# Optimization experiments

Measured on AMD Instinct MI355X. Metric: run time of the kernel, lower is better.

Reference implementation:

```python
import jax, jax.numpy as jnp
import numpy as np

D_MODEL, D_STATE, EXPAND, V, BATCH, L = 32, 16, 2, 19, 32, 256
D_INNER = EXPAND * D_MODEL          # 64
DT_RANK = 2                          # ceil(d_model/16)
N_NODES = BATCH * V                  # 608


def setup_inputs() -> dict:
    key = jax.random.key(0)
    ks = jax.random.split(key, 16)
    # 32 fully-connected directed 19-vertex graphs (no self loops), block-diagonal batching
    ii, jj = np.nonzero(~np.eye(V, dtype=bool))
    offs = (np.arange(BATCH) * V)[:, None]
    src = (ii[None, :] + offs).reshape(-1)
    dst = (jj[None, :] + offs).reshape(-1)
    edge_index = jnp.asarray(np.stack([src, dst]), dtype=jnp.int32)  # (2, 10944)
    E = edge_index.shape[1]
    # dt_proj bias init (inverse softplus of dt in [dt_min, dt_max]), as in the torch module
    dt = jnp.exp(jax.random.uniform(ks[6], (D_INNER,)) * (np.log(0.1) - np.log(0.001)) + np.log(0.001))
    dt = jnp.maximum(dt, 1e-4)
    inv_dt = dt + jnp.log(-jnp.expm1(-dt))
    s = 0.05
    return {
        'x_in': jax.random.normal(ks[0], (N_NODES, L, D_MODEL), jnp.float32),
        'edge_index': edge_index,
        'edge_weight': jax.random.uniform(ks[1], (E,), jnp.float32, 0.1, 1.0),
        'in_proj_w': jax.random.normal(ks[2], (2 * D_INNER, D_MODEL), jnp.float32) * s,
        'x_proj_w': jax.random.normal(ks[3], (DT_RANK + 2 * D_STATE, D_INNER), jnp.float32) * s,
        'dt_proj_w': jax.random.uniform(ks[4], (D_INNER, DT_RANK), jnp.float32, -DT_RANK ** -0.5, DT_RANK ** -0.5),
        'dt_proj_b': inv_dt,
        'A_log': jnp.log(jnp.broadcast_to(jnp.arange(1, D_STATE + 1, dtype=jnp.float32), (D_INNER, D_STATE))),
        'D_param': jnp.ones((D_INNER,), jnp.float32),
        'out_proj_w': jax.random.normal(ks[5], (D_MODEL, D_INNER), jnp.float32) * s,
        'gA_w': jax.random.normal(ks[7], (D_INNER, D_INNER), jnp.float32) * s,
        'gA_b': jnp.zeros((D_INNER,), jnp.float32),
        'gB_w': jax.random.normal(ks[8], (D_INNER, D_INNER), jnp.float32) * s,
        'gB_b': jnp.zeros((D_INNER,), jnp.float32),
        'gC_w': jax.random.normal(ks[9], (D_INNER, D_INNER), jnp.float32) * s,
        'gC_b': jnp.zeros((D_INNER,), jnp.float32),
    }


def reference(x_in, edge_index, edge_weight, in_proj_w, x_proj_w, dt_proj_w,
              dt_proj_b, A_log, D_param, out_proj_w,
              gA_w, gA_b, gB_w, gB_b, gC_w, gC_b):
    n_nodes, seqlen, _ = x_in.shape
    dt_rank = dt_proj_w.shape[1]
    d_state = A_log.shape[1]

    # --- GCN symmetric normalization with self loops (weight 1), as in PyG GCNConv ---
    loop = jnp.arange(n_nodes, dtype=edge_index.dtype)
    src = jnp.concatenate([edge_index[0], loop])
    dst = jnp.concatenate([edge_index[1], loop])
    w = jnp.concatenate([edge_weight, jnp.ones((n_nodes,), edge_weight.dtype)])
    deg = jax.ops.segment_sum(w, dst, num_segments=n_nodes)
    dinv = jax.lax.rsqrt(jnp.maximum(deg, 1e-12))
    norm = w * dinv[src] * dinv[dst]  # (E+n,)

    def gcn_vec(f, W, b):  # f: (V, d)
        h = f @ W.T
        return jax.ops.segment_sum(norm[:, None] * h[src], dst, num_segments=n_nodes) + b

    def gcn_state(f, W, b):  # f: (V, d, n); linear acts on the d (feature) axis
        h = jnp.einsum('vdn,ed->ven', f, W)
        agg = jax.ops.segment_sum(norm[:, None, None] * h[src], dst, num_segments=n_nodes)
        return agg + b[None, :, None]

    # --- projections ---
    xz = jnp.einsum('vld,ed->vle', x_in, in_proj_w)            # (V, L, 2*d_inner)
    x, z = jnp.split(xz, 2, axis=-1)                           # (V, L, d_inner)
    x_dbl = jnp.einsum('vld,ed->vle', x, x_proj_w)
    dtr, Bm, Cm = jnp.split(x_dbl, [dt_rank, dt_rank + d_state], axis=-1)
    dt = jax.nn.softplus(jnp.einsum('vlr,dr->vld', dtr, dt_proj_w) + dt_proj_b)  # (V, L, d_inner)
    A = -jnp.exp(A_log)                                        # (d_inner, d_state)

    # --- selective scan with per-timestep GCN on state (A), input (B), output (C) ---
    def step(s, inp):
        dt_t, B_t, C_t, u_t, z_t = inp  # (V,d), (V,n), (V,n), (V,d), (V,d)
        dA = jnp.exp(dt_t[:, :, None] * A[None])               # (V, d, n)
        sA = gcn_state(s, gA_w, gA_b)
        uB = gcn_vec(u_t, gB_w, gB_b)                          # (V, d)
        s_new = sA * dA + uB[:, :, None] * (dt_t[:, :, None] * B_t[:, None, :])
        sC = gcn_state(s_new, gC_w, gC_b)
        y_t = jnp.einsum('vdn,vn->vd', sC, C_t) + D_param * u_t
        y_t = y_t * jax.nn.silu(z_t)
        return s_new, y_t

    xs = (dt.transpose(1, 0, 2), Bm.transpose(1, 0, 2), Cm.transpose(1, 0, 2),
          x.transpose(1, 0, 2), z.transpose(1, 0, 2))
    s0 = jnp.zeros((n_nodes, A_log.shape[0], d_state), x_in.dtype)
    _, ys = jax.lax.scan(step, s0, xs)                         # (L, V, d_inner)
    y = ys.transpose(1, 0, 2)                                  # (V, L, d_inner)
    return jnp.einsum('vle,oe->vlo', y, out_proj_w)            # (V, L, d_model)
```

## Files before the change

kernel.cpp:

```cpp
#include <hip/hip_runtime.h>
#include <hip/hip_bf16.h>

typedef __hip_bfloat16 bf16;
typedef unsigned short ushort_t;
typedef __attribute__((ext_vector_type(8))) short bf16x8;
typedef __attribute__((ext_vector_type(4))) float f32x4;

#define NV_   19
#define NB_   32
#define NN_   608
#define LL_   256
#define NE_   10944
#define NROWS (NN_*LL_)
#define NTOT  (NROWS*64)
#define NBC   (NROWS*16)

__device__ __forceinline__ float b2f(bf16 x){ return __bfloat162float(x); }
__device__ __forceinline__ bf16 f2b(float x){ return __float2bfloat16(x); }
__device__ __forceinline__ unsigned short f2bs(float x){
  union { float f; unsigned u; } c; c.f = x;
  unsigned r = c.u + 0x7FFFu + ((c.u >> 16) & 1u);
  return (unsigned short)(r >> 16);
}
__device__ __forceinline__ float busf(unsigned short s){
  union { unsigned u; float f; } c; c.u = ((unsigned)s) << 16; return c.f;
}
__device__ __forceinline__ unsigned pkrn(float a, float b){
  union { __hip_bfloat162 h2; unsigned u; } c;
  float2 t; t.x = a; t.y = b;
  c.h2 = __float22bfloat162_rn(t);
  return c.u;
}
__device__ __forceinline__ float blo(unsigned u){
  union { unsigned x; float f; } c; c.x = u << 16; return c.f;
}
__device__ __forceinline__ float bhi(unsigned u){
  union { unsigned x; float f; } c; c.x = u & 0xffff0000u; return c.f;
}
__device__ __forceinline__ float softplusf(float x){
  return fmaxf(x, 0.f) + log1pf(expf(-fabsf(x)));
}

__global__ void k_deg(const int* __restrict__ ei, const float* __restrict__ ew,
                      float* __restrict__ deg){
  int i = blockIdx.x*256 + threadIdx.x;
  if (i < NN_) atomicAdd(&deg[i], 1.0f);
  if (i < NE_) atomicAdd(&deg[ei[NE_ + i]], ew[i]);
}

__global__ void k_dinv(const float* __restrict__ deg, float* __restrict__ dinv,
                       float* __restrict__ M){
  int v = blockIdx.x*256 + threadIdx.x;
  if (v >= NN_) return;
  float r = rsqrtf(fmaxf(deg[v], 1e-12f));
  dinv[v] = r;
  int b = v / NV_, lv = v - b*NV_;
  M[(b*NV_ + lv)*NV_ + lv] = r*r;
}

__global__ void k_edges(const int* __restrict__ ei, const float* __restrict__ ew,
                        const float* __restrict__ dinv, float* __restrict__ M){
  int i = blockIdx.x*256 + threadIdx.x;
  if (i >= NE_) return;
  int s = ei[i], d = ei[NE_ + i];
  float nrm = ew[i] * dinv[s] * dinv[d];
  int b = d / NV_;
  atomicAdd(&M[(b*NV_ + (d - b*NV_))*NV_ + (s - b*NV_)], nrm);
}

__global__ __launch_bounds__(256)
void k_proj(const float* __restrict__ xin, const float* __restrict__ inw,
            const float* __restrict__ xpw,
            bf16* __restrict__ u, bf16* __restrict__ zs,
            float* __restrict__ dtr, bf16* __restrict__ Bm, bf16* __restrict__ Cm){
  __shared__ float inT[32*129];
  __shared__ float xpT[64*35];
  __shared__ float xl[2][4][32];
  __shared__ float xh[2][4][64];
  int tid = threadIdx.x;
  for (int i = tid; i < 128*32; i += 256){
    int e = i >> 5, d = i & 31;
    inT[d*129 + e] = inw[i];
  }
  for (int i = tid; i < 34*64; i += 256){
    int j = i >> 6, e = i & 63;
    xpT[e*35 + j] = xpw[i];
  }
  int w = tid >> 6, lane = tid & 63;
  for (int rg = 0; rg < 32; rg++){
    int p = rg & 1;
    int r = (blockIdx.x*32 + rg)*4 + w;
    if (lane < 32) xl[p][w][lane] = xin[r*32 + lane];
    __syncthreads();
    float a0 = 0.f, a1 = 0.f;
    #pragma unroll
    for (int d = 0; d < 32; d++){
      float xv = xl[p][w][d];
      a0 = fmaf(inT[d*129 + lane], xv, a0);
      a1 = fmaf(inT[d*129 + 64 + lane], xv, a1);
    }
    int node = r >> 8, l = r & 255;
    long ob = (long)l*NN_ + node;
    u[ob*64 + lane] = f2b(a0);
    zs[ob*64 + lane] = f2b(a1 / (1.f + expf(-a1)));
    xh[p][w][lane] = a0;
    __syncthreads();
    if (lane < 34){
      float acc = 0.f;
      #pragma unroll
      for (int e = 0; e < 64; e++) acc = fmaf(xpT[e*35 + lane], xh[p][w][e], acc);
      if (lane < 2)       dtr[ob*2 + lane] = acc;
      else if (lane < 18) Bm[ob*16 + lane - 2] = f2b(acc);
      else                Cm[ob*16 + lane - 18] = f2b(acc);
    }
  }
}

__global__ __launch_bounds__(256)
void k_ub(const bf16* __restrict__ u, const float* __restrict__ gBw,
          const float* __restrict__ gBb, const float* __restrict__ Mg,
          const float* __restrict__ dtrg, const float* __restrict__ dtw,
          const float* __restrict__ dtb,
          bf16* __restrict__ uBsp, bf16* __restrict__ spb){
  __shared__ float wT[64*65];
  __shared__ float uL[19*64];
  __shared__ float hL[20*64];
  __shared__ float MLP[640];
  int b = blockIdx.x & 31, tc = blockIdx.x >> 5;
  int tid = threadIdx.x;
  for (int i = tid; i < 4096; i += 256){
    int e = i >> 6, d = i & 63;
    wT[d*65 + e] = gBw[i];
  }
  for (int i = tid; i < 640; i += 256){
    int vp = i >> 5, c = i & 31, g = c >> 3, k = c & 7;
    int v = g + 4*k;
    MLP[i] = (k < 5 && vp < 19 && v < 19) ? Mg[b*361 + v*19 + vp] : 0.f;
  }
  int vg = tid >> 6, e = tid & 63;
  int v0 = vg, v1 = vg+4, v2 = vg+8, v3 = vg+12, v4 = vg+16;
  int v4c = (vg == 3) ? 18 : v4;
  float w0e = dtw[e*2], w1e = dtw[e*2 + 1], dbe = dtb[e], bbe = gBb[e];
  const float* mlb = MLP + vg*8;
  for (int tt = 0; tt < 8; tt++){
    int t = tc*8 + tt;
    long rb = (long)t*NN_ + b*19;
    const bf16* up = u + rb*64;
    for (int i = tid; i < 1216; i += 256) uL[i] = b2f(up[i]);
    __syncthreads();
    float h0=0.f,h1=0.f,h2=0.f,h3=0.f,h4=0.f;
    #pragma unroll
    for (int d = 0; d < 64; d++){
      float wv = wT[d*65 + e];
      h0 = fmaf(wv, uL[v0*64 + d], h0);
      h1 = fmaf(wv, uL[v1*64 + d], h1);
      h2 = fmaf(wv, uL[v2*64 + d], h2);
      h3 = fmaf(wv, uL[v3*64 + d], h3);
      h4 = fmaf(wv, uL[v4c*64 + d], h4);
    }
    hL[v0*64 + e] = h0; hL[v1*64 + e] = h1; hL[v2*64 + e] = h2;
    hL[v3*64 + e] = h3; hL[v4*64 + e] = h4;
    __syncthreads();
    float acc0=bbe, acc1=bbe, acc2=bbe, acc3=bbe, acc4=bbe;
    #pragma unroll
    for (int vp = 0; vp < 20; vp++){
      float hv = hL[vp*64 + e];
      float4 m4 = *(const float4*)(mlb + vp*32);
      float  m5 = mlb[vp*32 + 4];
      acc0 = fmaf(m4.x, hv, acc0); acc1 = fmaf(m4.y, hv, acc1);
      acc2 = fmaf(m4.z, hv, acc2); acc3 = fmaf(m4.w, hv, acc3);
      acc4 = fmaf(m5,  hv, acc4);
    }
    float2 q0 = *(const float2*)(dtrg + (rb+v0)*2);
    float2 q1 = *(const float2*)(dtrg + (rb+v1)*2);
    float2 q2 = *(const float2*)(dtrg + (rb+v2)*2);
    float2 q3 = *(const float2*)(dtrg + (rb+v3)*2);
    float2 q4 = *(const float2*)(dtrg + (rb+v4c)*2);
    float s0 = softplusf(fmaf(q0.x, w0e, fmaf(q0.y, w1e, dbe)));
    float s1 = softplusf(fmaf(q1.x, w0e, fmaf(q1.y, w1e, dbe)));
    float s2 = softplusf(fmaf(q2.x, w0e, fmaf(q2.y, w1e, dbe)));
    float s3 = softplusf(fmaf(q3.x, w0e, fmaf(q3.y, w1e, dbe)));
    float s4 = softplusf(fmaf(q4.x, w0e, fmaf(q4.y, w1e, dbe)));
    bf16* op = uBsp + rb*64;
    bf16* sp = spb + rb*64;
    op[v0*64 + e] = f2b(acc0*s0);  sp[v0*64 + e] = f2b(s0);
    op[v1*64 + e] = f2b(acc1*s1);  sp[v1*64 + e] = f2b(s1);
    op[v2*64 + e] = f2b(acc2*s2);  sp[v2*64 + e] = f2b(s2);
    op[v3*64 + e] = f2b(acc3*s3);  sp[v3*64 + e] = f2b(s3);
    if (vg != 3){ op[v4*64 + e] = f2b(acc4*s4); sp[v4*64 + e] = f2b(s4); }
    __syncthreads();
  }
}

__global__ __launch_bounds__(1024)
void k_scan(const float* __restrict__ Mg,
            const bf16* __restrict__ spbg, const bf16* __restrict__ uBspg,
            const bf16* __restrict__ Bg, const bf16* __restrict__ Cg,
            const float* __restrict__ gAw, const float* __restrict__ gAb,
            const float* __restrict__ gCw, const float* __restrict__ gCb,
            const float* __restrict__ Alog, bf16* __restrict__ yp)
{
  __shared__ __align__(16) short Sb[2*32*72];
  __shared__ __align__(16) short H0[2*64*40];
  __shared__ __align__(16) short H1[2*64*40];
  __shared__ __align__(16) short Yx[2][32*64];
  int b = blockIdx.x >> 3, npair = blockIdx.x & 7;
  int tid = threadIdx.x;
  int team = tid >> 9;
  int tw   = (tid >> 6) & 7;
  int lane = tid & 63;
  int l15  = lane & 15, quad = lane >> 4;
  int n = npair*2 + team;
  int mt = tw >> 2, nt = tw & 3;
  int et = tw >> 1, vt = tw & 1;

  for (int i = tid; i < 2304; i += 1024) ((int*)Sb)[i] = 0;

  bf16x8 wa0, wa1, wc0, wc1;
  {
    #define PACK8(dst, p) { float4 lo_ = *(const float4*)(p); \
      float4 hi_ = *(const float4*)((p)+4); \
      dst[0]=(short)f2bs(lo_.x); dst[1]=(short)f2bs(lo_.y); \
      dst[2]=(short)f2bs(lo_.z); dst[3]=(short)f2bs(lo_.w); \
      dst[4]=(short)f2bs(hi_.x); dst[5]=(short)f2bs(hi_.y); \
      dst[6]=(short)f2bs(hi_.z); dst[7]=(short)f2bs(hi_.w); }
    const float* wrA = gAw + (16*nt + l15)*64 + quad*8;
    const float* wrC = gCw + (16*nt + l15)*64 + quad*8;
    PACK8(wa0, wrA) PACK8(wa1, wrA + 32)
    PACK8(wc0, wrC) PACK8(wc1, wrC + 32)
    #undef PACK8
  }
  bf16x8 mf;
  {
    const float* mb = Mg + b*361;
    int vr = 16*vt + l15; if (vr > 18) vr = 18;
    #pragma unroll
    for (int j = 0; j < 8; j++){
      int vp = quad*8 + j;
      mf[j] = (short)f2bs((vp < 19) ? mb[vr*19 + vp] : 0.f);
    }
  }
  int e0 = 16*et + 4*quad;
  int v_ = 16*vt + l15;
  int vc = (v_ > 18) ? 18 : v_;
  bool vok = (v_ < 19);
  float4 gab = *(const float4*)(gAb + e0);
  float4 gcb = *(const float4*)(gCb + e0);
  float An0 = -__expf(Alog[(e0+0)*16 + n]);
  float An1 = -__expf(Alog[(e0+1)*16 + n]);
  float An2 = -__expf(Alog[(e0+2)*16 + n]);
  float An3 = -__expf(Alog[(e0+3)*16 + n]);

  short* Sme  = Sb + team*32*72;
  short* H0me = H0 + team*64*40;
  short* H1me = H1 + team*64*40;
  int nodeBase = b*19;
  const short* prS  = Sme + (16*mt + l15)*72 + quad*8;
  short*       pwH0 = H0me + (16*nt + l15)*40 + 16*mt + quad*4;
  short*       pwH1 = H1me + (16*nt + l15)*40 + 16*mt + quad*4;
  const short* arH0 = H0me + (16*et + l15)*40 + quad*8;
  const short* arH1 = H1me + (16*et + l15)*40 + quad*8;
  short*       swS  = Sme + v_*72 + e0;

  long row0 = (long)nodeBase + vc;
  const ushort_t* psp = (const ushort_t*)spbg  + row0*64 + e0;
  const ushort_t* pub = (const ushort_t*)uBspg + row0*64 + e0;
  const ushort_t* pB  = (const ushort_t*)Bg + row0*16 + n;
  const ushort_t* pC  = (const ushort_t*)Cg + row0*16 + n;
  uint2 sp_n = *(const uint2*)psp;
  uint2 ub_n = *(const uint2*)pub;
  float B_n = busf(*pB);
  float C_b2 = busf(*pC);
  float C_a = 0.f;
  float pyo0=0.f,pyo1=0.f,pyo2=0.f,pyo3=0.f;
  float pyn0=0.f,pyn1=0.f,pyn2=0.f,pyn3=0.f;

  __syncthreads();
  {
    bf16x8 a0 = *(const bf16x8*)prS;
    bf16x8 a1 = *(const bf16x8*)(prS + 32);
    f32x4 p = {0.f,0.f,0.f,0.f};
    p = __builtin_amdgcn_mfma_f32_16x16x32_bf16(a0, wa0, p, 0,0,0);
    p = __builtin_amdgcn_mfma_f32_16x16x32_bf16(a1, wa1, p, 0,0,0);
    uint2 h; h.x = pkrn(p[0], p[1]); h.y = pkrn(p[2], p[3]);
    *(uint2*)pwH0 = h;
  }
  __syncthreads();

  for (int t = 0; t < 256; t++){
    uint2 sp_u = sp_n, ub_u = ub_n; float B_u = B_n;
    psp += NN_*64; pub += NN_*64; pB += NN_*16; pC += NN_*16;
    sp_n = *(const uint2*)psp;
    ub_n = *(const uint2*)pub;
    B_n = busf(*pB);
    float C_t = busf(*pC);
    bf16x8 hf0 = *(const bf16x8*)arH0;
    bf16x8 hf1 = *(const bf16x8*)arH1;
    {
      f32x4 qa = {gab.x, gab.y, gab.z, gab.w};
      qa = __builtin_amdgcn_mfma_f32_16x16x32_bf16(hf0, mf, qa, 0,0,0);
      float dA0 = __expf(blo(sp_u.x)*An0);
      float dA1 = __expf(bhi(sp_u.x)*An1);
      float dA2 = __expf(blo(sp_u.y)*An2);
      float dA3 = __expf(bhi(sp_u.y)*An3);
      float x0 = fmaf(qa[0], dA0, blo(ub_u.x)*B_u);
      float x1 = fmaf(qa[1], dA1, bhi(ub_u.x)*B_u);
      float x2 = fmaf(qa[2], dA2, blo(ub_u.y)*B_u);
      float x3 = fmaf(qa[3], dA3, bhi(ub_u.y)*B_u);
      uint2 sv; sv.x = pkrn(x0, x1); sv.y = pkrn(x2, x3);
      *(uint2*)swS = sv;
    }
    if (team == 0 && t >= 2 && vok){
      uint2 yv = *(const uint2*)(&Yx[t & 1][v_*64 + e0]);
      uint2 ov;
      ov.x = pkrn(pyo0 + blo(yv.x), pyo1 + bhi(yv.x));
      ov.y = pkrn(pyo2 + blo(yv.y), pyo3 + bhi(yv.y));
      *(uint2*)(yp + (((long)npair*256 + (t-2))*NN_ + nodeBase + v_)*64 + e0) = ov;
    }
    if (t >= 1){
      f32x4 qc = {gcb.x, gcb.y, gcb.z, gcb.w};
      qc = __builtin_amdgcn_mfma_f32_16x16x32_bf16(hf1, mf, qc, 0,0,0);
      float y0 = qc[0]*C_a, y1 = qc[1]*C_a, y2 = qc[2]*C_a, y3 = qc[3]*C_a;
      if (team == 1){
        uint2 yv; yv.x = pkrn(y0, y1); yv.y = pkrn(y2, y3);
        *(uint2*)(&Yx[(t-1) & 1][v_*64 + e0]) = yv;
      } else {
        pyo0 = pyn0; pyo1 = pyn1; pyo2 = pyn2; pyo3 = pyn3;
        pyn0 = y0; pyn1 = y1; pyn2 = y2; pyn3 = y3;
      }
    }
    C_a = C_b2; C_b2 = C_t;
    __syncthreads();
    {
      bf16x8 a0 = *(const bf16x8*)prS;
      bf16x8 a1 = *(const bf16x8*)(prS + 32);
      f32x4 p = {0.f,0.f,0.f,0.f};
      p = __builtin_amdgcn_mfma_f32_16x16x32_bf16(a0, wc0, p, 0,0,0);
      p = __builtin_amdgcn_mfma_f32_16x16x32_bf16(a1, wc1, p, 0,0,0);
      uint2 h; h.x = pkrn(p[0], p[1]); h.y = pkrn(p[2], p[3]);
      *(uint2*)pwH1 = h;
      f32x4 r = {0.f,0.f,0.f,0.f};
      r = __builtin_amdgcn_mfma_f32_16x16x32_bf16(a0, wa0, r, 0,0,0);
      r = __builtin_amdgcn_mfma_f32_16x16x32_bf16(a1, wa1, r, 0,0,0);
      uint2 g; g.x = pkrn(r[0], r[1]); g.y = pkrn(r[2], r[3]);
      *(uint2*)pwH0 = g;
    }
    __syncthreads();
  }
  {
    bf16x8 hf1 = *(const bf16x8*)arH1;
    f32x4 qc = {gcb.x, gcb.y, gcb.z, gcb.w};
    qc = __builtin_amdgcn_mfma_f32_16x16x32_bf16(hf1, mf, qc, 0,0,0);
    float y0 = qc[0]*C_a, y1 = qc[1]*C_a, y2 = qc[2]*C_a, y3 = qc[3]*C_a;
    if (team == 1){
      uint2 yv; yv.x = pkrn(y0, y1); yv.y = pkrn(y2, y3);
      *(uint2*)(&Yx[1][v_*64 + e0]) = yv;
    } else {
      pyo0 = pyn0; pyo1 = pyn1; pyo2 = pyn2; pyo3 = pyn3;
      pyn0 = y0; pyn1 = y1; pyn2 = y2; pyn3 = y3;
    }
  }
  __syncthreads();
  if (team == 0 && vok){
    uint2 yv = *(const uint2*)(&Yx[0][v_*64 + e0]);
    uint2 ov;
    ov.x = pkrn(pyo0 + blo(yv.x), pyo1 + bhi(yv.x));
    ov.y = pkrn(pyo2 + blo(yv.y), pyo3 + bhi(yv.y));
    *(uint2*)(yp + (((long)npair*256 + 254)*NN_ + nodeBase + v_)*64 + e0) = ov;
    uint2 yw = *(const uint2*)(&Yx[1][v_*64 + e0]);
    uint2 o2;
    o2.x = pkrn(pyn0 + blo(yw.x), pyn1 + bhi(yw.x));
    o2.y = pkrn(pyn2 + blo(yw.y), pyn3 + bhi(yw.y));
    *(uint2*)(yp + (((long)npair*256 + 255)*NN_ + nodeBase + v_)*64 + e0) = o2;
  }
}

__global__ __launch_bounds__(256)
void k_final(const bf16* __restrict__ yp, const bf16* __restrict__ u,
             const bf16* __restrict__ zs, const float* __restrict__ Dp,
             const float* __restrict__ ow, float* __restrict__ out)
{
  __shared__ float oT[64*33];
  __shared__ float yl[2][4][64];
  int tid = threadIdx.x;
  for (int i = tid; i < 32*64; i += 256){
    int o = i >> 6, e = i & 63;
    oT[e*33 + o] = ow[i];
  }
  int w = tid >> 6, lane = tid & 63;
  float dpl = Dp[lane];
  for (int rg = 0; rg < 16; rg++){
    int p = rg & 1;
    long r = (long)(blockIdx.x*16 + rg)*4 + w;
    long base = r*64;
    float y = dpl * b2f(u[base + lane]);
    #pragma unroll
    for (int q = 0; q < 8; q++) y += b2f(yp[(long)q*NTOT + base + lane]);
    y *= b2f(zs[base + lane]);
    yl[p][w][lane] = y;
    __syncthreads();
    if (lane < 32){
      float acc = 0.f;
      #pragma unroll
      for (int e = 0; e < 64; e++) acc = fmaf(oT[e*33 + lane], yl[p][w][e], acc);
      int t = (int)(r / NN_), node = (int)(r - (long)t*NN_);
      out[((long)node*256 + t)*32 + lane] = acc;
    }
  }
}

extern "C" void kernel_launch(void* const* d_in, const int* in_sizes, int n_in,
                              void* d_out, int out_size, void* d_ws, size_t ws_size,
                              hipStream_t stream)
{
  (void)in_sizes; (void)n_in; (void)out_size; (void)ws_size;
  const float* xin = (const float*)d_in[0];
  const int*   ei  = (const int*)  d_in[1];
  const float* ew  = (const float*)d_in[2];
  const float* inw = (const float*)d_in[3];
  const float* xpw = (const float*)d_in[4];
  const float* dtw = (const float*)d_in[5];
  const float* dtb = (const float*)d_in[6];
  const float* Alog= (const float*)d_in[7];
  const float* Dp  = (const float*)d_in[8];
  const float* ow  = (const float*)d_in[9];
  const float* gAw = (const float*)d_in[10];
  const float* gAb = (const float*)d_in[11];
  const float* gBw = (const float*)d_in[12];
  const float* gBb = (const float*)d_in[13];
  const float* gCw = (const float*)d_in[14];
  const float* gCb = (const float*)d_in[15];
  float* out = (float*)d_out;

  float* Mg   = (float*)d_ws;
  float* deg  = Mg + 11552;
  float* dinv = deg + 608;
  float* dtr  = dinv + 608;
  bf16*  u    = (bf16*)(dtr + 2*NROWS);
  bf16*  zs   = u + NTOT;
  bf16*  uBsp = zs + NTOT;
  bf16*  Bm   = uBsp + NTOT;
  bf16*  Cm   = Bm + NBC;
  bf16*  spb  = Cm + NBC;
  bf16*  yp   = spb + NTOT;

  hipMemsetAsync(d_ws, 0, (11552 + 608)*sizeof(float), stream);
  k_deg  <<<(NE_ + 255)/256, 256, 0, stream>>>(ei, ew, deg);
  k_dinv <<<(NN_ + 255)/256, 256, 0, stream>>>(deg, dinv, Mg);
  k_edges<<<(NE_ + 255)/256, 256, 0, stream>>>(ei, ew, dinv, Mg);
  k_proj <<<NROWS/(4*32), 256, 0, stream>>>(xin, inw, xpw, u, zs, dtr, Bm, Cm);
  k_ub   <<<32*32, 256, 0, stream>>>(u, gBw, gBb, Mg, dtr, dtw, dtb, uBsp, spb);
  k_scan <<<NB_*8, 1024, 0, stream>>>(Mg, spb, uBsp, Bm, Cm, gAw, gAb, gCw, gCb,
                                      Alog, yp);
  k_final<<<NROWS/(4*16), 256, 0, stream>>>(yp, u, zs, Dp, ow, out);
}
```

Baseline: 704.4 us.

## Shrink scan block to one wavefront per state index, removing intra-team barriers

The scan kernel drops from 1024 threads (8 waves per state index) to 128 threads, where one wavefront handles a whole state index and loops over all tiles in registers. Most shared-memory handoffs become intra-wave, leaving a single barrier per timestep for exchanging partial y sums between the two waves. The goal is to cut per-step synchronisation latency in the serial scan recurrence. The cost is far more MFMA and exp work per wave plus higher register pressure, with only 256 small blocks left to fill the GPU.

```diff
diff --git a/kernel.cpp b/kernel.cpp
--- a/kernel.cpp
+++ b/kernel.cpp
@@ -192,7 +192,7 @@
   }
 }
 
-__global__ __launch_bounds__(1024)
+__global__ __launch_bounds__(128, 1)
 void k_scan(const float* __restrict__ Mg,
             const bf16* __restrict__ spbg, const bf16* __restrict__ uBspg,
             const bf16* __restrict__ Bg, const bf16* __restrict__ Cg,
@@ -200,178 +200,212 @@
             const float* __restrict__ gCw, const float* __restrict__ gCb,
             const float* __restrict__ Alog, bf16* __restrict__ yp)
 {
-  __shared__ __align__(16) short Sb[2*32*72];
-  __shared__ __align__(16) short H0[2*64*40];
-  __shared__ __align__(16) short H1[2*64*40];
-  __shared__ __align__(16) short Yx[2][32*64];
-  int b = blockIdx.x >> 3, npair = blockIdx.x & 7;
-  int tid = threadIdx.x;
-  int team = tid >> 9;
-  int tw   = (tid >> 6) & 7;
-  int lane = tid & 63;
-  int l15  = lane & 15, quad = lane >> 4;
-  int n = npair*2 + team;
-  int mt = tw >> 2, nt = tw & 3;
-  int et = tw >> 1, vt = tw & 1;
-
-  for (int i = tid; i < 2304; i += 1024) ((int*)Sb)[i] = 0;
-
-  bf16x8 wa0, wa1, wc0, wc1;
-  {
-    #define PACK8(dst, p) { float4 lo_ = *(const float4*)(p); \
-      float4 hi_ = *(const float4*)((p)+4); \
-      dst[0]=(short)f2bs(lo_.x); dst[1]=(short)f2bs(lo_.y); \
-      dst[2]=(short)f2bs(lo_.z); dst[3]=(short)f2bs(lo_.w); \
-      dst[4]=(short)f2bs(hi_.x); dst[5]=(short)f2bs(hi_.y); \
-      dst[6]=(short)f2bs(hi_.z); dst[7]=(short)f2bs(hi_.w); }
-    const float* wrA = gAw + (16*nt + l15)*64 + quad*8;
-    const float* wrC = gCw + (16*nt + l15)*64 + quad*8;
-    PACK8(wa0, wrA) PACK8(wa1, wrA + 32)
-    PACK8(wc0, wrC) PACK8(wc1, wrC + 32)
-    #undef PACK8
-  }
-  bf16x8 mf;
+  __shared__ __align__(16) short Sb[2][32*72];
+  __shared__ __align__(16) short Hb0[2][64*40];
+  __shared__ __align__(16) short Hb1[2][64*40];
+  __shared__ __align__(16) unsigned Yex[2][2][64*12];
+
+  const int b = blockIdx.x >> 3, npair = blockIdx.x & 7;
+  const int tid = threadIdx.x;
+  const int team = tid >> 6;
+  const int lane = tid & 63;
+  const int l15 = lane & 15, quad = lane >> 4;
+  const int n = npair*2 + team;
+
+  for (int i = tid; i < 2560; i += 128) ((int*)Hb0)[i] = 0;
+
+  short* S  = Sb[team];
+  short* h0 = Hb0[team];
+  short* h1 = Hb1[team];
+
+  bf16x8 wa[4][2], wc[4][2];
+  #pragma unroll
+  for (int nt = 0; nt < 4; nt++){
+    const float* ra = gAw + (16*nt + l15)*64 + quad*8;
+    const float* rc = gCw + (16*nt + l15)*64 + quad*8;
+    #pragma unroll
+    for (int kc = 0; kc < 2; kc++){
+      #pragma unroll
+      for (int j = 0; j < 8; j++){
+        wa[nt][kc][j] = (short)f2bs(ra[kc*32 + j]);
+        wc[nt][kc][j] = (short)f2bs(rc[kc*32 + j]);
+      }
+    }
+  }
+  bf16x8 mfT[2];
   {
     const float* mb = Mg + b*361;
-    int vr = 16*vt + l15; if (vr > 18) vr = 18;
-    #pragma unroll
-    for (int j = 0; j < 8; j++){
-      int vp = quad*8 + j;
-      mf[j] = (short)f2bs((vp < 19) ? mb[vr*19 + vp] : 0.f);
-    }
-  }
-  int e0 = 16*et + 4*quad;
-  int v_ = 16*vt + l15;
-  int vc = (v_ > 18) ? 18 : v_;
-  bool vok = (v_ < 19);
-  float4 gab = *(const float4*)(gAb + e0);
-  float4 gcb = *(const float4*)(gCb + e0);
-  float An0 = -__expf(Alog[(e0+0)*16 + n]);
-  float An1 = -__expf(Alog[(e0+1)*16 + n]);
-  float An2 = -__expf(Alog[(e0+2)*16 + n]);
-  float An3 = -__expf(Alog[(e0+3)*16 + n]);
-
-  short* Sme  = Sb + team*32*72;
-  short* H0me = H0 + team*64*40;
-  short* H1me = H1 + team*64*40;
-  int nodeBase = b*19;
-  const short* prS  = Sme + (16*mt + l15)*72 + quad*8;
-  short*       pwH0 = H0me + (16*nt + l15)*40 + 16*mt + quad*4;
-  short*       pwH1 = H1me + (16*nt + l15)*40 + 16*mt + quad*4;
-  const short* arH0 = H0me + (16*et + l15)*40 + quad*8;
-  const short* arH1 = H1me + (16*et + l15)*40 + quad*8;
-  short*       swS  = Sme + v_*72 + e0;
-
-  long row0 = (long)nodeBase + vc;
-  const ushort_t* psp = (const ushort_t*)spbg  + row0*64 + e0;
-  const ushort_t* pub = (const ushort_t*)uBspg + row0*64 + e0;
-  const ushort_t* pB  = (const ushort_t*)Bg + row0*16 + n;
-  const ushort_t* pC  = (const ushort_t*)Cg + row0*16 + n;
-  uint2 sp_n = *(const uint2*)psp;
-  uint2 ub_n = *(const uint2*)pub;
-  float B_n = busf(*pB);
-  float C_b2 = busf(*pC);
-  float C_a = 0.f;
-  float pyo0=0.f,pyo1=0.f,pyo2=0.f,pyo3=0.f;
-  float pyn0=0.f,pyn1=0.f,pyn2=0.f,pyn3=0.f;
+    #pragma unroll
+    for (int vt = 0; vt < 2; vt++){
+      int v = 16*vt + l15;
+      #pragma unroll
+      for (int j = 0; j < 8; j++){
+        int vp = quad*8 + j;
+        mfT[vt][j] = (short)f2bs((v < 19 && vp < 19) ? mb[v*19 + vp] : 0.f);
+      }
+    }
+  }
+  float anv[4][4], gabv[4][4], gcbv[4][4];
+  #pragma unroll
+  for (int et = 0; et < 4; et++){
+    #pragma unroll
+    for (int r = 0; r < 4; r++){
+      int e = 16*et + 4*quad + r;
+      anv[et][r]  = -__expf(Alog[e*16 + n]);
+      gabv[et][r] = gAb[e];
+      gcbv[et][r] = gCb[e];
+    }
+  }
+
+  const int v1 = 16 + l15;
+  const int v1c = (v1 > 18) ? 18 : v1;
+  const long r0 = (long)b*19 + l15;
+  const long r1 = (long)b*19 + v1c;
+  const char* psp0 = (const char*)spbg  + r0*128 + quad*8;
+  const char* psp1 = (const char*)spbg  + r1*128 + quad*8;
+  const char* pub0 = (const char*)uBspg + r0*128 + quad*8;
+  const char* pub1 = (const char*)uBspg + r1*128 + quad*8;
+  const ushort_t* pB0 = (const ushort_t*)Bg + r0*16 + n;
+  const ushort_t* pB1 = (const ushort_t*)Bg + r1*16 + n;
+  const ushort_t* pC0 = (const ushort_t*)Cg + r0*16 + n;
+  const ushort_t* pC1 = (const ushort_t*)Cg + r1*16 + n;
+  bf16* py0 = yp + ((long)npair*256*NN_ + (long)b*19 + l15)*64;
+  bf16* py1 = yp + ((long)npair*256*NN_ + (long)b*19 + v1)*64;
+  const int ebase = (team == 0) ? 0 : 2;
+
+  uint2 sp2[2][4], ub2[2][4];
+  #pragma unroll
+  for (int et = 0; et < 4; et++){
+    sp2[0][et] = *(const uint2*)(psp0 + 32*et);
+    sp2[1][et] = *(const uint2*)(psp1 + 32*et);
+    ub2[0][et] = *(const uint2*)(pub0 + 32*et);
+    ub2[1][et] = *(const uint2*)(pub1 + 32*et);
+  }
+  float Bu0 = busf(*pB0), Bu1 = busf(*pB1);
+  float Cu0 = busf(*pC0), Cu1 = busf(*pC1);
 
   __syncthreads();
-  {
-    bf16x8 a0 = *(const bf16x8*)prS;
-    bf16x8 a1 = *(const bf16x8*)(prS + 32);
-    f32x4 p = {0.f,0.f,0.f,0.f};
-    p = __builtin_amdgcn_mfma_f32_16x16x32_bf16(a0, wa0, p, 0,0,0);
-    p = __builtin_amdgcn_mfma_f32_16x16x32_bf16(a1, wa1, p, 0,0,0);
-    uint2 h; h.x = pkrn(p[0], p[1]); h.y = pkrn(p[2], p[3]);
-    *(uint2*)pwH0 = h;
-  }
-  __syncthreads();
+  bf16x8 hf[4];
+  #pragma unroll
+  for (int et = 0; et < 4; et++)
+    hf[et] = *(const bf16x8*)(h0 + (16*et + l15)*40 + quad*8);
 
   for (int t = 0; t < 256; t++){
-    uint2 sp_u = sp_n, ub_u = ub_n; float B_u = B_n;
-    psp += NN_*64; pub += NN_*64; pB += NN_*16; pC += NN_*16;
-    sp_n = *(const uint2*)psp;
-    ub_n = *(const uint2*)pub;
-    B_n = busf(*pB);
-    float C_t = busf(*pC);
-    bf16x8 hf0 = *(const bf16x8*)arH0;
-    bf16x8 hf1 = *(const bf16x8*)arH1;
+    #pragma unroll
+    for (int vt = 0; vt < 2; vt++){
+      float Bu = vt ? Bu1 : Bu0;
+      #pragma unroll
+      for (int et = 0; et < 4; et++){
+        f32x4 qa = {gabv[et][0], gabv[et][1], gabv[et][2], gabv[et][3]};
+        qa = __builtin_amdgcn_mfma_f32_16x16x32_bf16(hf[et], mfT[vt], qa, 0,0,0);
+        uint2 s_ = sp2[vt][et], u_ = ub2[vt][et];
+        float x0 = fmaf(qa[0], __expf(blo(s_.x)*anv[et][0]), blo(u_.x)*Bu);
+        float x1 = fmaf(qa[1], __expf(bhi(s_.x)*anv[et][1]), bhi(u_.x)*Bu);
+        float x2 = fmaf(qa[2], __expf(blo(s_.y)*anv[et][2]), blo(u_.y)*Bu);
+        float x3 = fmaf(qa[3], __expf(bhi(s_.y)*anv[et][3]), bhi(u_.y)*Bu);
+        uint2 sv; sv.x = pkrn(x0,x1); sv.y = pkrn(x2,x3);
+        *(uint2*)(S + (16*vt + l15)*72 + 16*et + 4*quad) = sv;
+      }
+    }
+    psp0 += NN_*128; psp1 += NN_*128; pub0 += NN_*128; pub1 += NN_*128;
+    pB0 += NN_*16; pB1 += NN_*16; pC0 += NN_*16; pC1 += NN_*16;
+    #pragma unroll
+    for (int et = 0; et < 4; et++){
+      sp2[0][et] = *(const uint2*)(psp0 + 32*et);
+      sp2[1][et] = *(const uint2*)(psp1 + 32*et);
+      ub2[0][et] = *(const uint2*)(pub0 + 32*et);
+      ub2[1][et] = *(const uint2*)(pub1 + 32*et);
+    }
+    Bu0 = busf(*pB0); Bu1 = busf(*pB1);
+    float Cn0 = busf(*pC0), Cn1 = busf(*pC1);
+    bf16x8 a0[2], a1[2];
+    #pragma unroll
+    for (int mt = 0; mt < 2; mt++){
+      a0[mt] = *(const bf16x8*)(S + (16*mt + l15)*72 + quad*8);
+      a1[mt] = *(const bf16x8*)(S + (16*mt + l15)*72 + 32 + quad*8);
+    }
+    #pragma unroll
+    for (int nt = 0; nt < 4; nt++){
+      #pragma unroll
+      for (int mt = 0; mt < 2; mt++){
+        f32x4 p = {0.f,0.f,0.f,0.f};
+        p = __builtin_amdgcn_mfma_f32_16x16x32_bf16(a0[mt], wc[nt][0], p, 0,0,0);
+        p = __builtin_amdgcn_mfma_f32_16x16x32_bf16(a1[mt], wc[nt][1], p, 0,0,0);
+        uint2 h; h.x = pkrn(p[0],p[1]); h.y = pkrn(p[2],p[3]);
+        *(uint2*)(h1 + (16*nt + l15)*40 + 16*mt + 4*quad) = h;
+      }
+    }
+    #pragma unroll
+    for (int nt = 0; nt < 4; nt++){
+      #pragma unroll
+      for (int mt = 0; mt < 2; mt++){
+        f32x4 p = {0.f,0.f,0.f,0.f};
+        p = __builtin_amdgcn_mfma_f32_16x16x32_bf16(a0[mt], wa[nt][0], p, 0,0,0);
+        p = __builtin_amdgcn_mfma_f32_16x16x32_bf16(a1[mt], wa[nt][1], p, 0,0,0);
+        uint2 h; h.x = pkrn(p[0],p[1]); h.y = pkrn(p[2],p[3]);
+        *(uint2*)(h0 + (16*nt + l15)*40 + 16*mt + 4*quad) = h;
+      }
+    }
+    #pragma unroll
+    for (int et = 0; et < 4; et++)
+      hf[et] = *(const bf16x8*)(h0 + (16*et + l15)*40 + quad*8);
+    float yk[2][2][4];
+    uint4 ys0, ys1;
+    #pragma unroll
+    for (int et = 0; et < 4; et++){
+      bf16x8 hc = *(const bf16x8*)(h1 + (16*et + l15)*40 + quad*8);
+      #pragma unroll
+      for (int vt = 0; vt < 2; vt++){
+        float Cv = vt ? Cu1 : Cu0;
+        f32x4 qc = {gcbv[et][0], gcbv[et][1], gcbv[et][2], gcbv[et][3]};
+        qc = __builtin_amdgcn_mfma_f32_16x16x32_bf16(hc, mfT[vt], qc, 0,0,0);
+        float y0_ = qc[0]*Cv, y1_ = qc[1]*Cv, y2_ = qc[2]*Cv, y3_ = qc[3]*Cv;
+        if ((et < 2) == (team == 0)){
+          yk[vt][et & 1][0] = y0_; yk[vt][et & 1][1] = y1_;
+          yk[vt][et & 1][2] = y2_; yk[vt][et & 1][3] = y3_;
+        } else {
+          if (vt == 0){
+            if ((et & 1) == 0){ ys0.x = pkrn(y0_,y1_); ys0.y = pkrn(y2_,y3_); }
+            else              { ys0.z = pkrn(y0_,y1_); ys0.w = pkrn(y2_,y3_); }
+          } else {
+            if ((et & 1) == 0){ ys1.x = pkrn(y0_,y1_); ys1.y = pkrn(y2_,y3_); }
+            else              { ys1.z = pkrn(y0_,y1_); ys1.w = pkrn(y2_,y3_); }
+          }
+        }
+      }
+    }
     {
-      f32x4 qa = {gab.x, gab.y, gab.z, gab.w};
-      qa = __builtin_amdgcn_mfma_f32_16x16x32_bf16(hf0, mf, qa, 0,0,0);
-      float dA0 = __expf(blo(sp_u.x)*An0);
-      float dA1 = __expf(bhi(sp_u.x)*An1);
-      float dA2 = __expf(blo(sp_u.y)*An2);
-      float dA3 = __expf(bhi(sp_u.y)*An3);
-      float x0 = fmaf(qa[0], dA0, blo(ub_u.x)*B_u);
-      float x1 = fmaf(qa[1], dA1, bhi(ub_u.x)*B_u);
-      float x2 = fmaf(qa[2], dA2, blo(ub_u.y)*B_u);
-      float x3 = fmaf(qa[3], dA3, bhi(ub_u.y)*B_u);
-      uint2 sv; sv.x = pkrn(x0, x1); sv.y = pkrn(x2, x3);
-      *(uint2*)swS = sv;
-    }
-    if (team == 0 && t >= 2 && vok){
-      uint2 yv = *(const uint2*)(&Yx[t & 1][v_*64 + e0]);
-      uint2 ov;
-      ov.x = pkrn(pyo0 + blo(yv.x), pyo1 + bhi(yv.x));
-      ov.y = pkrn(pyo2 + blo(yv.y), pyo3 + bhi(yv.y));
-      *(uint2*)(yp + (((long)npair*256 + (t-2))*NN_ + nodeBase + v_)*64 + e0) = ov;
-    }
-    if (t >= 1){
-      f32x4 qc = {gcb.x, gcb.y, gcb.z, gcb.w};
-      qc = __builtin_amdgcn_mfma_f32_16x16x32_bf16(hf1, mf, qc, 0,0,0);
-      float y0 = qc[0]*C_a, y1 = qc[1]*C_a, y2 = qc[2]*C_a, y3 = qc[3]*C_a;
-      if (team == 1){
-        uint2 yv; yv.x = pkrn(y0, y1); yv.y = pkrn(y2, y3);
-        *(uint2*)(&Yx[(t-1) & 1][v_*64 + e0]) = yv;
-      } else {
-        pyo0 = pyn0; pyo1 = pyn1; pyo2 = pyn2; pyo3 = pyn3;
-        pyn0 = y0; pyn1 = y1; pyn2 = y2; pyn3 = y3;
-      }
-    }
-    C_a = C_b2; C_b2 = C_t;
+      unsigned* dst = &Yex[team][t & 1][lane*12];
+      *(uint4*)(dst)     = ys0;
+      *(uint4*)(dst + 4) = ys1;
+    }
     __syncthreads();
     {
-      bf16x8 a0 = *(const bf16x8*)prS;
-      bf16x8 a1 = *(const bf16x8*)(prS + 32);
-      f32x4 p = {0.f,0.f,0.f,0.f};
-      p = __builtin_amdgcn_mfma_f32_16x16x32_bf16(a0, wc0, p, 0,0,0);
-      p = __builtin_amdgcn_mfma_f32_16x16x32_bf16(a1, wc1, p, 0,0,0);
-      uint2 h; h.x = pkrn(p[0], p[1]); h.y = pkrn(p[2], p[3]);
-      *(uint2*)pwH1 = h;
-      f32x4 r = {0.f,0.f,0.f,0.f};
-      r = __builtin_amdgcn_mfma_f32_16x16x32_bf16(a0, wa0, r, 0,0,0);
-      r = __builtin_amdgcn_mfma_f32_16x16x32_bf16(a1, wa1, r, 0,0,0);
-      uint2 g; g.x = pkrn(r[0], r[1]); g.y = pkrn(r[2], r[3]);
-      *(uint2*)pwH0 = g;
-    }
-    __syncthreads();
-  }
-  {
-    bf16x8 hf1 = *(const bf16x8*)arH1;
-    f32x4 qc = {gcb.x, gcb.y, gcb.z, gcb.w};
-    qc = __builtin_amdgcn_mfma_f32_16x16x32_bf16(hf1, mf, qc, 0,0,0);
-    float y0 = qc[0]*C_a, y1 = qc[1]*C_a, y2 = qc[2]*C_a, y3 = qc[3]*C_a;
-    if (team == 1){
-      uint2 yv; yv.x = pkrn(y0, y1); yv.y = pkrn(y2, y3);
-      *(uint2*)(&Yx[1][v_*64 + e0]) = yv;
-    } else {
-      pyo0 = pyn0; pyo1 = pyn1; pyo2 = pyn2; pyo3 = pyn3;
-      pyn0 = y0; pyn1 = y1; pyn2 = y2; pyn3 = y3;
-    }
-  }
-  __syncthreads();
-  if (team == 0 && vok){
-    uint2 yv = *(const uint2*)(&Yx[0][v_*64 + e0]);
-    uint2 ov;
-    ov.x = pkrn(pyo0 + blo(yv.x), pyo1 + bhi(yv.x));
-    ov.y = pkrn(pyo2 + blo(yv.y), pyo3 + bhi(yv.y));
-    *(uint2*)(yp + (((long)npair*256 + 254)*NN_ + nodeBase + v_)*64 + e0) = ov;
-    uint2 yw = *(const uint2*)(&Yx[1][v_*64 + e0]);
-    uint2 o2;
-    o2.x = pkrn(pyn0 + blo(yw.x), pyn1 + bhi(yw.x));
-    o2.y = pkrn(pyn2 + blo(yw.y), pyn3 + bhi(yw.y));
-    *(uint2*)(yp + (((long)npair*256 + 255)*NN_ + nodeBase + v_)*64 + e0) = o2;
+      const unsigned* src = &Yex[team ^ 1][t & 1][lane*12];
+      uint4 g0 = *(const uint4*)(src);
+      uint4 g1 = *(const uint4*)(src + 4);
+      #pragma unroll
+      for (int vt = 0; vt < 2; vt++){
+        uint4 g = vt ? g1 : g0;
+        unsigned o0 = pkrn(yk[vt][0][0] + blo(g.x), yk[vt][0][1] + bhi(g.x));
+        unsigned o1 = pkrn(yk[vt][0][2] + blo(g.y), yk[vt][0][3] + bhi(g.y));
+        unsigned o2 = pkrn(yk[vt][1][0] + blo(g.z), yk[vt][1][1] + bhi(g.z));
+        unsigned o3 = pkrn(yk[vt][1][2] + blo(g.w), yk[vt][1][3] + bhi(g.w));
+        if (vt == 0){
+          uint2 w0; w0.x = o0; w0.y = o1;
+          uint2 w1; w1.x = o2; w1.y = o3;
+          *(uint2*)(py0 + 16*ebase + 4*quad)       = w0;
+          *(uint2*)(py0 + 16*(ebase+1) + 4*quad)   = w1;
+        } else if (l15 < 3){
+          uint2 w0; w0.x = o0; w0.y = o1;
+          uint2 w1; w1.x = o2; w1.y = o3;
+          *(uint2*)(py1 + 16*ebase + 4*quad)       = w0;
+          *(uint2*)(py1 + 16*(ebase+1) + 4*quad)   = w1;
+        }
+      }
+      py0 += (long)NN_*64; py1 += (long)NN_*64;
+      Cu0 = Cn0; Cu1 = Cn1;
+    }
   }
 }
 
@@ -450,7 +484,7 @@
   k_edges<<<(NE_ + 255)/256, 256, 0, stream>>>(ei, ew, dinv, Mg);
   k_proj <<<NROWS/(4*32), 256, 0, stream>>>(xin, inw, xpw, u, zs, dtr, Bm, Cm);
   k_ub   <<<32*32, 256, 0, stream>>>(u, gBw, gBb, Mg, dtr, dtw, dtb, uBsp, spb);
-  k_scan <<<NB_*8, 1024, 0, stream>>>(Mg, spb, uBsp, Bm, Cm, gAw, gAb, gCw, gCb,
-                                      Alog, yp);
+  k_scan <<<NB_*8, 128, 0, stream>>>(Mg, spb, uBsp, Bm, Cm, gAw, gAb, gCw, gCb,
+                                     Alog, yp);
   k_final<<<NROWS/(4*16), 256, 0, stream>>>(yp, u, zs, Dp, ow, out);
 }
```

Result: slower. 970.7 us (+37.8%).
